# Performance work log

Measured on AMD Instinct MI355X. Metric: run time of the kernel, lower is better.

Reference implementation:

```python
import jax, jax.numpy as jnp
import numpy as np

# FP4 (E2M1) code table: nibble = [sign(1) | exp(2) | mantissa(1)]
# magnitudes for codes 0..7: 0, 0.5, 1, 1.5, 2, 3, 4, 6; codes 8..15 are negated.
_MAG = np.array([0.0, 0.5, 1.0, 1.5, 2.0, 3.0, 4.0, 6.0], dtype=np.float32)
FP4_LUT = jnp.asarray(np.concatenate([_MAG, -_MAG]))  # [16]

BLOCK = 16  # scale-factor block size along in_features


def setup_inputs() -> dict:
    key = jax.random.key(0)
    k0, k1, k2, k3, k4 = jax.random.split(key, 5)
    M, K, N = 32, 8192, 8192  # tokens, in_features, out_features
    inp = jax.random.normal(k0, (M, K), dtype=jnp.float32)
    qweight = jax.random.randint(k1, (N, K // 2), 0, 256, dtype=jnp.int32)  # packed FP4 pairs
    scales = jax.random.uniform(k2, (N, K // BLOCK), dtype=jnp.float32)      # per-block scales
    amax = jax.random.uniform(k3, (1,), dtype=jnp.float32) + 0.5             # global scale
    bias = jax.random.normal(k4, (N,), dtype=jnp.float32)
    return {"input": inp, "qweight": qweight, "scales": scales, "amax": amax, "bias": bias}


def _dequantize(qweight, scales, amax):
    N = qweight.shape[0]
    low = qweight & 0xF            # first element of each pair
    high = (qweight >> 4) & 0xF    # second element
    nibbles = jnp.stack([low, high], axis=-1).reshape(N, -1)  # [N, K]
    vals = FP4_LUT[nibbles]                                   # [N, K] fp4 values
    # per-block scaling: block of BLOCK contiguous in-features shares one scale
    w = (vals.reshape(N, -1, BLOCK) * scales[..., None]).reshape(N, -1)
    return w * amax[0]


def reference(input, qweight, scales, amax, bias):
    weight = _dequantize(qweight, scales, amax)   # [N, K] full-precision weight
    return input @ weight.T + bias                # F.linear
```

## Files before the change

### kernel.cpp

```cpp
#include <hip/hip_runtime.h>
#include <hip/hip_bf16.h>

#define M_DIM 32
#define K_DIM 8192
#define N_DIM 8192
#define KS 16
#define KCH (K_DIM / KS)
#define CHK 128
#define NCHK (KCH / CHK)
#define STEPS (CHK / 32)
#define NPB 128
#define NBLK (N_DIM / NPB)
#define MAIN_BLOCKS (NBLK * KS)

#define QW_ROW (K_DIM / 8)
#define SC_ROW (K_DIM / 16)

#define QROW 17
#define AROW 136
#define SROW 9

typedef _Float16 half8   __attribute__((ext_vector_type(8)));
typedef _Float16 half4_t __attribute__((ext_vector_type(4)));
typedef _Float16 half2_t __attribute__((ext_vector_type(2)));
typedef float    floatx4 __attribute__((ext_vector_type(4)));

#if defined(__has_builtin)
#if __has_builtin(__builtin_amdgcn_cvt_scalef32_pk_f16_fp4)
#define HAVE_CVT_FP4 1
#endif
#endif

#ifndef HAVE_CVT_FP4
__device__ __forceinline__ uint32_t dec2(uint32_t q) {
  uint32_t c0 = q & 0xFu, c1 = (q >> 4) & 0xFu;
  uint32_t m0 = c0 & 7u, m1 = c1 & 7u;
  uint32_t t0 = min(28u * m0, m0 + 28u);
  uint32_t t1 = min(28u * m1, m1 + 28u);
  return (t0 << 9) | ((c0 & 8u) << 12)
       | (t1 << 25) | ((c1 & 8u) << 28);
}
#endif

__device__ __forceinline__ half8 decode8(int4 q, float scale) {
  union { uint32_t u[4]; half2_t h2[4]; half8 h; } w;
#ifdef HAVE_CVT_FP4
  w.h2[0] = __builtin_amdgcn_cvt_scalef32_pk_f16_fp4((unsigned)q.x, 1.0f, 0);
  w.h2[1] = __builtin_amdgcn_cvt_scalef32_pk_f16_fp4((unsigned)q.y, 1.0f, 0);
  w.h2[2] = __builtin_amdgcn_cvt_scalef32_pk_f16_fp4((unsigned)q.z, 1.0f, 0);
  w.h2[3] = __builtin_amdgcn_cvt_scalef32_pk_f16_fp4((unsigned)q.w, 1.0f, 0);
#else
  w.u[0] = dec2((uint32_t)q.x);
  w.u[1] = dec2((uint32_t)q.y);
  w.u[2] = dec2((uint32_t)q.z);
  w.u[3] = dec2((uint32_t)q.w);
#endif
  _Float16 s = (_Float16)scale;
  half8 sv = {s, s, s, s, s, s, s, s};
  return w.h * sv;
}

__global__ void init_out_kernel(floatx4* __restrict__ out4,
                                const floatx4* __restrict__ bias4) {
  int idx = blockIdx.x * blockDim.x + threadIdx.x;
  out4[idx] = bias4[idx & (N_DIM / 4 - 1)];
}

__global__ void reduce_kernel(const floatx4* __restrict__ part,
                              const floatx4* __restrict__ bias4,
                              floatx4* __restrict__ out4) {
  int idx = blockIdx.x * blockDim.x + threadIdx.x;
  floatx4 acc = bias4[idx & (N_DIM / 4 - 1)];
#pragma unroll
  for (int s = 0; s < KS; ++s)
    acc += part[(size_t)s * (M_DIM * N_DIM / 4) + idx];
  out4[idx] = acc;
}

template <bool PARTIAL>
__global__ __launch_bounds__(256, 3) void fp4_linear_kernel(
    const float* __restrict__ inp,
    const int4*  __restrict__ qw4,
    const float* __restrict__ scales,
    const float* __restrict__ amaxp,
    float* __restrict__ outp)
{
  __shared__ int4     Qs[NPB * QROW];
  __shared__ _Float16 As[M_DIM * AROW];
  __shared__ float    Ss[NPB * SROW];

  const int t    = threadIdx.x;
  const int lane = t & 63;
  const int w    = t >> 6;
  const int ks   = blockIdx.x & (KS - 1);
  const int nb   = blockIdx.x >> 4;
  const int n0   = nb * NPB;
  const int kb   = ks * KCH;
  const float amax = amaxp[0];

  int4    qreg[8];
  floatx4 areg[4];
  floatx4 sreg;

  auto load_chunk = [&](int kc) {
    const int4* qbase = qw4 + (kc >> 3);
#pragma unroll
    for (int p = 0; p < 8; ++p) {
      const int r = p * 16 + (t >> 4);
      qreg[p] = qbase[(size_t)(n0 + r) * QW_ROW + (t & 15)];
    }
    const float* abase = inp + kc;
#pragma unroll
    for (int p = 0; p < 4; ++p) {
      const int r = p * 8 + (t >> 5);
      areg[p] = ((const floatx4*)(abase + (size_t)r * K_DIM))[t & 31];
    }
    sreg = ((const floatx4*)(scales + (size_t)(n0 + (t >> 1)) * SC_ROW
                             + (kc >> 4)))[t & 1];
  };

  auto store_chunk = [&]() {
#pragma unroll
    for (int p = 0; p < 8; ++p)
      Qs[(p * 16 + (t >> 4)) * QROW + (t & 15)] = qreg[p];
#pragma unroll
    for (int p = 0; p < 4; ++p) {
      floatx4 f = areg[p];
      half4_t h;
      h[0] = (_Float16)f[0]; h[1] = (_Float16)f[1];
      h[2] = (_Float16)f[2]; h[3] = (_Float16)f[3];
      *(half4_t*)&As[(p * 8 + (t >> 5)) * AROW + (t & 31) * 4] = h;
    }
    float* sd = &Ss[(t >> 1) * SROW + (t & 1) * 4];
    sd[0] = sreg[0] * amax; sd[1] = sreg[1] * amax;
    sd[2] = sreg[2] * amax; sd[3] = sreg[3] * amax;
  };

  const int row  = lane & 15;
  const int quad = lane >> 4;
  const int nloc = w * 32;

  floatx4 acc00 = {0.f, 0.f, 0.f, 0.f};
  floatx4 acc01 = {0.f, 0.f, 0.f, 0.f};
  floatx4 acc10 = {0.f, 0.f, 0.f, 0.f};
  floatx4 acc11 = {0.f, 0.f, 0.f, 0.f};

  const int4*     qApt = &Qs[(nloc + row) * QROW];
  const int4*     qBpt = &Qs[(nloc + 16 + row) * QROW];
  const _Float16* a0pt = &As[row * AROW];
  const _Float16* a1pt = &As[(row + 16) * AROW];
  const float*    sApt = &Ss[(nloc + row) * SROW];
  const float*    sBpt = &Ss[(nloc + 16 + row) * SROW];

  load_chunk(kb);
  for (int c = 0; c < NCHK; ++c) {
    if (c) __syncthreads();
    store_chunk();
    __syncthreads();
    if (c + 1 < NCHK) load_chunk(kb + (c + 1) * CHK);

#pragma unroll
    for (int it = 0; it < STEPS; ++it) {
      const int qi  = it * 4 + quad;
      const int kbl = it * 2 + (quad >> 1);
      const int klo = it * 32 + quad * 8;
      half8 bA = decode8(qApt[qi], sApt[kbl]);
      half8 bB = decode8(qBpt[qi], sBpt[kbl]);
      half8 a0 = *(const half8*)(a0pt + klo);
      half8 a1 = *(const half8*)(a1pt + klo);
      acc00 = __builtin_amdgcn_mfma_f32_16x16x32_f16(a0, bA, acc00, 0, 0, 0);
      acc01 = __builtin_amdgcn_mfma_f32_16x16x32_f16(a0, bB, acc01, 0, 0, 0);
      acc10 = __builtin_amdgcn_mfma_f32_16x16x32_f16(a1, bA, acc10, 0, 0, 0);
      acc11 = __builtin_amdgcn_mfma_f32_16x16x32_f16(a1, bB, acc11, 0, 0, 0);
    }
  }

  if (PARTIAL) {
    float* pb = outp + (size_t)ks * (M_DIM * N_DIM);
#pragma unroll
    for (int r = 0; r < 4; ++r) {
      const int m = quad * 4 + r;
      float* o0 = pb + (size_t)m * N_DIM + n0 + nloc;
      float* o1 = pb + (size_t)(m + 16) * N_DIM + n0 + nloc;
      o0[row]      = acc00[r];
      o0[16 + row] = acc01[r];
      o1[row]      = acc10[r];
      o1[16 + row] = acc11[r];
    }
  } else {
#pragma unroll
    for (int r = 0; r < 4; ++r) {
      const int m = quad * 4 + r;
      float* o0 = outp + (size_t)m * N_DIM + n0 + nloc;
      float* o1 = outp + (size_t)(m + 16) * N_DIM + n0 + nloc;
      unsafeAtomicAdd(o0 + row,      acc00[r]);
      unsafeAtomicAdd(o0 + 16 + row, acc01[r]);
      unsafeAtomicAdd(o1 + row,      acc10[r]);
      unsafeAtomicAdd(o1 + 16 + row, acc11[r]);
    }
  }
}

extern "C" void kernel_launch(void* const* d_in, const int* in_sizes, int n_in,
                              void* d_out, int out_size, void* d_ws, size_t ws_size,
                              hipStream_t stream) {
  const float* inp    = (const float*)d_in[0];
  const int4*  qw4    = (const int4*)d_in[1];
  const float* scales = (const float*)d_in[2];
  const float* amaxp  = (const float*)d_in[3];
  const float* bias   = (const float*)d_in[4];
  float* out = (float*)d_out;

  const size_t part_bytes = (size_t)KS * M_DIM * N_DIM * sizeof(float);
  if (ws_size >= part_bytes) {
    float* part = (float*)d_ws;
    fp4_linear_kernel<true><<<MAIN_BLOCKS, 256, 0, stream>>>(
        inp, qw4, scales, amaxp, part);
    reduce_kernel<<<M_DIM * N_DIM / 4 / 256, 256, 0, stream>>>(
        (const floatx4*)part, (const floatx4*)bias, (floatx4*)out);
  } else {
    init_out_kernel<<<M_DIM * N_DIM / 4 / 256, 256, 0, stream>>>(
        (floatx4*)out, (const floatx4*)bias);
    fp4_linear_kernel<false><<<MAIN_BLOCKS, 256, 0, stream>>>(
        inp, qw4, scales, amaxp, out);
  }
}
```

Measured before the change: 242.6 us.

## Load whole K-slice into shared memory once and pack int32 nibble bytes

Replaces the chunked double-buffered loop with a single up-front load of each block's full K-slice (weights, activations, scales) into LDS, followed by one barrier and a fully unrolled MFMA loop. Each packed int32 weight's low byte is compacted into a 4-byte word, which shrinks the LDS footprint. Scales are premultiplied by amax and stored as fp16. The hardware fp4 convert builtin is dropped in favour of the bit-trick decoder. The aim is to cut per-chunk barriers and let loads issue in larger batches. The cost is more LDS per block, lower occupancy (launch bounds 3 to 2), no overlap between loading and compute, and fp16 rounding of the scale products.

Measured after the change: 224.4 us. 1.08x faster.

```diff
diff --git a/kernel.cpp b/kernel.cpp
--- a/kernel.cpp
+++ b/kernel.cpp
@@ -6,56 +6,37 @@
 #define N_DIM 8192
 #define KS 16
 #define KCH (K_DIM / KS)
-#define CHK 128
-#define NCHK (KCH / CHK)
-#define STEPS (CHK / 32)
+#define STEPS (KCH / 32)
 #define NPB 128
 #define NBLK (N_DIM / NPB)
 #define MAIN_BLOCKS (NBLK * KS)
 
-#define QW_ROW (K_DIM / 8)
+#define QW_ROWI4 (K_DIM / 8)
 #define SC_ROW (K_DIM / 16)
 
-#define QROW 17
-#define AROW 136
-#define SROW 9
+#define QROW 65
+#define AROW 520
+#define SROW 34
 
 typedef _Float16 half8   __attribute__((ext_vector_type(8)));
 typedef _Float16 half4_t __attribute__((ext_vector_type(4)));
-typedef _Float16 half2_t __attribute__((ext_vector_type(2)));
 typedef float    floatx4 __attribute__((ext_vector_type(4)));
 
-#if defined(__has_builtin)
-#if __has_builtin(__builtin_amdgcn_cvt_scalef32_pk_f16_fp4)
-#define HAVE_CVT_FP4 1
-#endif
-#endif
-
-#ifndef HAVE_CVT_FP4
-__device__ __forceinline__ uint32_t dec2(uint32_t q) {
-  uint32_t c0 = q & 0xFu, c1 = (q >> 4) & 0xFu;
+__device__ __forceinline__ uint32_t dec2(uint32_t b) {
+  uint32_t c0 = b & 0xFu, c1 = (b >> 4) & 0xFu;
   uint32_t m0 = c0 & 7u, m1 = c1 & 7u;
   uint32_t t0 = min(28u * m0, m0 + 28u);
   uint32_t t1 = min(28u * m1, m1 + 28u);
   return (t0 << 9) | ((c0 & 8u) << 12)
        | (t1 << 25) | ((c1 & 8u) << 28);
 }
-#endif
-
-__device__ __forceinline__ half8 decode8(int4 q, float scale) {
-  union { uint32_t u[4]; half2_t h2[4]; half8 h; } w;
-#ifdef HAVE_CVT_FP4
-  w.h2[0] = __builtin_amdgcn_cvt_scalef32_pk_f16_fp4((unsigned)q.x, 1.0f, 0);
-  w.h2[1] = __builtin_amdgcn_cvt_scalef32_pk_f16_fp4((unsigned)q.y, 1.0f, 0);
-  w.h2[2] = __builtin_amdgcn_cvt_scalef32_pk_f16_fp4((unsigned)q.z, 1.0f, 0);
-  w.h2[3] = __builtin_amdgcn_cvt_scalef32_pk_f16_fp4((unsigned)q.w, 1.0f, 0);
-#else
-  w.u[0] = dec2((uint32_t)q.x);
-  w.u[1] = dec2((uint32_t)q.y);
-  w.u[2] = dec2((uint32_t)q.z);
-  w.u[3] = dec2((uint32_t)q.w);
-#endif
-  _Float16 s = (_Float16)scale;
+
+__device__ __forceinline__ half8 decode8p(uint32_t q, _Float16 s) {
+  union { uint32_t u[4]; half8 h; } w;
+  w.u[0] = dec2(q & 0xFFu);
+  w.u[1] = dec2((q >> 8) & 0xFFu);
+  w.u[2] = dec2((q >> 16) & 0xFFu);
+  w.u[3] = dec2((q >> 24) & 0xFFu);
   half8 sv = {s, s, s, s, s, s, s, s};
   return w.h * sv;
 }
@@ -78,16 +59,16 @@
 }
 
 template <bool PARTIAL>
-__global__ __launch_bounds__(256, 3) void fp4_linear_kernel(
+__global__ __launch_bounds__(256, 2) void fp4_linear_kernel(
     const float* __restrict__ inp,
     const int4*  __restrict__ qw4,
     const float* __restrict__ scales,
     const float* __restrict__ amaxp,
     float* __restrict__ outp)
 {
-  __shared__ int4     Qs[NPB * QROW];
+  __shared__ uint32_t Qs[NPB * QROW];
   __shared__ _Float16 As[M_DIM * AROW];
-  __shared__ float    Ss[NPB * SROW];
+  __shared__ _Float16 Ss[NPB * SROW];
 
   const int t    = threadIdx.x;
   const int lane = t & 63;
@@ -95,84 +76,100 @@
   const int ks   = blockIdx.x & (KS - 1);
   const int nb   = blockIdx.x >> 4;
   const int n0   = nb * NPB;
-  const int kb   = ks * KCH;
   const float amax = amaxp[0];
 
-  int4    qreg[8];
-  floatx4 areg[4];
-  floatx4 sreg;
-
-  auto load_chunk = [&](int kc) {
-    const int4* qbase = qw4 + (kc >> 3);
-#pragma unroll
-    for (int p = 0; p < 8; ++p) {
-      const int r = p * 16 + (t >> 4);
-      qreg[p] = qbase[(size_t)(n0 + r) * QW_ROW + (t & 15)];
-    }
-    const float* abase = inp + kc;
-#pragma unroll
-    for (int p = 0; p < 4; ++p) {
-      const int r = p * 8 + (t >> 5);
-      areg[p] = ((const floatx4*)(abase + (size_t)r * K_DIM))[t & 31];
-    }
-    sreg = ((const floatx4*)(scales + (size_t)(n0 + (t >> 1)) * SC_ROW
-                             + (kc >> 4)))[t & 1];
-  };
-
-  auto store_chunk = [&]() {
-#pragma unroll
-    for (int p = 0; p < 8; ++p)
-      Qs[(p * 16 + (t >> 4)) * QROW + (t & 15)] = qreg[p];
-#pragma unroll
-    for (int p = 0; p < 4; ++p) {
-      floatx4 f = areg[p];
+  {
+    const int4* qbase = qw4 + (size_t)ks * (KCH / 8);
+    for (int g = 0; g < 4; ++g) {
+      int4 tmp[8];
+#pragma unroll
+      for (int j = 0; j < 8; ++j) {
+        const int r = w * 32 + g * 8 + j;
+        tmp[j] = qbase[(size_t)(n0 + r) * QW_ROWI4 + lane];
+      }
+#pragma unroll
+      for (int j = 0; j < 8; ++j) {
+        const int r = w * 32 + g * 8 + j;
+        uint32_t pk = ((uint32_t)tmp[j].x & 0xFFu)
+                    | (((uint32_t)tmp[j].y & 0xFFu) << 8)
+                    | (((uint32_t)tmp[j].z & 0xFFu) << 16)
+                    | (((uint32_t)tmp[j].w & 0xFFu) << 24);
+        Qs[r * QROW + lane] = pk;
+      }
+    }
+  }
+
+  {
+    for (int g = 0; g < 2; ++g) {
+      floatx4 tmp[8];
+#pragma unroll
+      for (int j = 0; j < 4; ++j) {
+        const int r = w * 8 + g * 4 + j;
+        const floatx4* ab =
+            reinterpret_cast<const floatx4*>(inp + (size_t)r * K_DIM + ks * KCH);
+        tmp[2 * j]     = ab[lane];
+        tmp[2 * j + 1] = ab[lane + 64];
+      }
+#pragma unroll
+      for (int j = 0; j < 4; ++j) {
+        const int r = w * 8 + g * 4 + j;
+        floatx4 f0 = tmp[2 * j], f1 = tmp[2 * j + 1];
+        half4_t h0, h1;
+        h0[0] = (_Float16)f0[0]; h0[1] = (_Float16)f0[1];
+        h0[2] = (_Float16)f0[2]; h0[3] = (_Float16)f0[3];
+        h1[0] = (_Float16)f1[0]; h1[1] = (_Float16)f1[1];
+        h1[2] = (_Float16)f1[2]; h1[3] = (_Float16)f1[3];
+        *(half4_t*)&As[r * AROW + lane * 4]        = h0;
+        *(half4_t*)&As[r * AROW + (lane + 64) * 4] = h1;
+      }
+    }
+  }
+
+  {
+#pragma unroll
+    for (int j = 0; j < 4; ++j) {
+      const int idx = j * 256 + t;
+      const int r = idx >> 3, c = idx & 7;
+      floatx4 f = reinterpret_cast<const floatx4*>(
+          scales + (size_t)(n0 + r) * SC_ROW + ks * (KCH / 16))[c];
       half4_t h;
-      h[0] = (_Float16)f[0]; h[1] = (_Float16)f[1];
-      h[2] = (_Float16)f[2]; h[3] = (_Float16)f[3];
-      *(half4_t*)&As[(p * 8 + (t >> 5)) * AROW + (t & 31) * 4] = h;
-    }
-    float* sd = &Ss[(t >> 1) * SROW + (t & 1) * 4];
-    sd[0] = sreg[0] * amax; sd[1] = sreg[1] * amax;
-    sd[2] = sreg[2] * amax; sd[3] = sreg[3] * amax;
-  };
+      h[0] = (_Float16)(f[0] * amax); h[1] = (_Float16)(f[1] * amax);
+      h[2] = (_Float16)(f[2] * amax); h[3] = (_Float16)(f[3] * amax);
+      *(half4_t*)&Ss[r * SROW + c * 4] = h;
+    }
+  }
+  __syncthreads();
 
   const int row  = lane & 15;
   const int quad = lane >> 4;
   const int nloc = w * 32;
+
+  const uint32_t* qAp = &Qs[(nloc + row) * QROW];
+  const uint32_t* qBp = &Qs[(nloc + 16 + row) * QROW];
+  const _Float16* a0p = &As[row * AROW];
+  const _Float16* a1p = &As[(row + 16) * AROW];
+  const _Float16* sAp = &Ss[(nloc + row) * SROW];
+  const _Float16* sBp = &Ss[(nloc + 16 + row) * SROW];
 
   floatx4 acc00 = {0.f, 0.f, 0.f, 0.f};
   floatx4 acc01 = {0.f, 0.f, 0.f, 0.f};
   floatx4 acc10 = {0.f, 0.f, 0.f, 0.f};
   floatx4 acc11 = {0.f, 0.f, 0.f, 0.f};
 
-  const int4*     qApt = &Qs[(nloc + row) * QROW];
-  const int4*     qBpt = &Qs[(nloc + 16 + row) * QROW];
-  const _Float16* a0pt = &As[row * AROW];
-  const _Float16* a1pt = &As[(row + 16) * AROW];
-  const float*    sApt = &Ss[(nloc + row) * SROW];
-  const float*    sBpt = &Ss[(nloc + 16 + row) * SROW];
-
-  load_chunk(kb);
-  for (int c = 0; c < NCHK; ++c) {
-    if (c) __syncthreads();
-    store_chunk();
-    __syncthreads();
-    if (c + 1 < NCHK) load_chunk(kb + (c + 1) * CHK);
-
-#pragma unroll
-    for (int it = 0; it < STEPS; ++it) {
-      const int qi  = it * 4 + quad;
-      const int kbl = it * 2 + (quad >> 1);
-      const int klo = it * 32 + quad * 8;
-      half8 bA = decode8(qApt[qi], sApt[kbl]);
-      half8 bB = decode8(qBpt[qi], sBpt[kbl]);
-      half8 a0 = *(const half8*)(a0pt + klo);
-      half8 a1 = *(const half8*)(a1pt + klo);
-      acc00 = __builtin_amdgcn_mfma_f32_16x16x32_f16(a0, bA, acc00, 0, 0, 0);
-      acc01 = __builtin_amdgcn_mfma_f32_16x16x32_f16(a0, bB, acc01, 0, 0, 0);
-      acc10 = __builtin_amdgcn_mfma_f32_16x16x32_f16(a1, bA, acc10, 0, 0, 0);
-      acc11 = __builtin_amdgcn_mfma_f32_16x16x32_f16(a1, bB, acc11, 0, 0, 0);
-    }
+#pragma unroll
+  for (int it = 0; it < STEPS; ++it) {
+    const uint32_t qA = qAp[it * 4 + quad];
+    const uint32_t qB = qBp[it * 4 + quad];
+    const _Float16 sA = sAp[it * 2 + (quad >> 1)];
+    const _Float16 sB = sBp[it * 2 + (quad >> 1)];
+    half8 bA = decode8p(qA, sA);
+    half8 bB = decode8p(qB, sB);
+    half8 a0 = *(const half8*)(a0p + it * 32 + quad * 8);
+    half8 a1 = *(const half8*)(a1p + it * 32 + quad * 8);
+    acc00 = __builtin_amdgcn_mfma_f32_16x16x32_f16(a0, bA, acc00, 0, 0, 0);
+    acc01 = __builtin_amdgcn_mfma_f32_16x16x32_f16(a0, bB, acc01, 0, 0, 0);
+    acc10 = __builtin_amdgcn_mfma_f32_16x16x32_f16(a1, bA, acc10, 0, 0, 0);
+    acc11 = __builtin_amdgcn_mfma_f32_16x16x32_f16(a1, bB, acc11, 0, 0, 0);
   }
 
   if (PARTIAL) {
```
